# Performance work log

Hardware: AMD Instinct MI355X
Metric: run time of the kernel (lower is better)

Reference implementation:

```python
import jax, jax.numpy as jnp
import numpy as np

T, B, D, H, L = 512, 128, 256, 256, 4
EPS = 1e-5

def _ln(x, g, b):
    m = jnp.mean(x, axis=-1, keepdims=True)
    v = jnp.mean((x - m) ** 2, axis=-1, keepdims=True)
    return (x - m) * jax.lax.rsqrt(v + EPS) * g + b

def setup_inputs() -> dict:
    key = jax.random.key(0)
    ks = jax.random.split(key, 24)
    s = 0.02
    inp = {
        "x": jax.random.normal(ks[0], (T, B, D), dtype=jnp.float32),
        "lengths": jax.random.randint(ks[1], (B,), 1, T + 1, dtype=jnp.int32),
        # LinearEnchancedGRU params
        "Wr": jax.random.normal(ks[2], (D + H, H)) * s,
        "gr": jnp.ones((H,)), "br": jnp.zeros((H,)),
        "Wz": jax.random.normal(ks[3], (D + H, H)) * s,
        "gz": jnp.ones((H,)), "bz": jnp.zeros((H,)),
        "Wl": jax.random.normal(ks[4], (D + H, H)) * s,
        "gl": jnp.ones((H,)), "bl": jnp.zeros((H,)),
        "Wlt": jax.random.normal(ks[5], (D, H)) * s,
        "Cx": jax.random.normal(ks[6], (D, H)) * s,
        "Ch_w": jax.random.normal(ks[7], (H, H)) * s,
        "Ch_b": jnp.zeros((H,)),
        # TransitionGRU stack params [L, ...]
        "tWr": jax.random.normal(ks[8], (L, H, H)) * s,
        "tgr": jnp.ones((L, H)), "tbr": jnp.zeros((L, H)),
        "tWz": jax.random.normal(ks[9], (L, H, H)) * s,
        "tgz": jnp.ones((L, H)), "tbz": jnp.zeros((L, H)),
        "tWc": jax.random.normal(ks[10], (L, H, H)) * s,
        "tbc": jnp.zeros((L, H)),
    }
    return inp

def reference(x, lengths, Wr, gr, br, Wz, gz, bz, Wl, gl, bl, Wlt, Cx, Ch_w, Ch_b,
              tWr, tgr, tbr, tWz, tgz, tbz, tWc, tbc):
    # x: [T,B,D]; lengths: [B]. Packed-sequence semantics: hidden state of a
    # finished example is frozen; its outputs are zero padding.
    mask = jnp.arange(T, dtype=jnp.int32)[:, None] < lengths[None, :]  # [T,B]

    def cell(xt, h):
        cat = jnp.concatenate([xt, h], axis=-1)  # [B, D+H]
        r = jax.nn.sigmoid(_ln(cat @ Wr, gr, br))
        z = jax.nn.sigmoid(_ln(cat @ Wz, gz, bz))
        l = jax.nn.sigmoid(_ln(cat @ Wl, gl, bl))
        n = jnp.tanh(xt @ Cx + r * (h @ Ch_w + Ch_b)) + l * (xt @ Wlt)
        h = (1.0 - z) * h + z * n
        for i in range(L):  # deep transition stack (fixed small depth)
            ri = jax.nn.sigmoid(_ln(h @ tWr[i], tgr[i], tbr[i]))
            zi = jax.nn.sigmoid(_ln(h @ tWz[i], tgz[i], tbz[i]))
            ni = jnp.tanh(ri * (h @ tWc[i] + tbc[i]))
            h = (1.0 - zi) * ni + zi * h
        return h

    def step(h, inputs):
        xt, mt = inputs  # [B,D], [B]
        hn = cell(xt, h)
        hn = jnp.where(mt[:, None], hn, h)
        out = jnp.where(mt[:, None], hn, 0.0)
        return hn, out

    h0 = jnp.zeros((B, H), dtype=x.dtype)
    _, outs = jax.lax.scan(step, h0, (x, mask))  # outs: [T,B,H]
    return outs
```

## Files before the change

### kernel.cpp

```cpp
#include <hip/hip_runtime.h>
#include <hip/hip_bf16.h>

#define T_ 512
#define B_ 128
#define D_ 256
#define H_ 256
#define EPS 1e-5f

typedef __attribute__((ext_vector_type(8))) short short8;
typedef __attribute__((ext_vector_type(4))) short short4v;
typedef __attribute__((ext_vector_type(4))) float f32x4;

#define WT1A_OFF 0
#define WT1B_OFF 393216
#define WT1C_OFF 524288
#define WTT_OFF  589824
#define WTT_PER  196608
#define WT_TOTAL 1376256

#define PRE_OFFB  2752512UL
#define SLOT_OFFB 4325376UL
#define NSLOTS    256

__device__ __forceinline__ short f2bf(float f) {
  unsigned u = __builtin_bit_cast(unsigned, f);
  u = (u + 0x7FFFu + ((u >> 16) & 1u)) >> 16;
  return (short)u;
}

__device__ __forceinline__ f32x4 zero4() { f32x4 z = {0.f, 0.f, 0.f, 0.f}; return z; }

__device__ __forceinline__ f32x4 mfma16(short8 a, short8 b, f32x4 c) {
  return __builtin_amdgcn_mfma_f32_16x16x32_bf16(a, b, c, 0, 0, 0);
}

__device__ __forceinline__ void red2(float& a, float& b) {
  #pragma unroll
  for (int off = 32; off; off >>= 1) {
    a += __shfl_xor(a, off);
    b += __shfl_xor(b, off);
  }
}

__device__ __forceinline__ f32x4 ln_sig(f32x4 v, f32x4 g, f32x4 bb) {
  float s1 = v[0] + v[1] + v[2] + v[3];
  float s2 = v[0]*v[0] + v[1]*v[1] + v[2]*v[2] + v[3]*v[3];
  red2(s1, s2);
  float m = s1 * (1.f / 256.f);
  float var = s2 * (1.f / 256.f) - m * m;
  float rs = rsqrtf((var > 0.f ? var : 0.f) + EPS);
  f32x4 o;
  #pragma unroll
  for (int i = 0; i < 4; ++i) {
    float t = (v[i] - m) * rs * g[i] + bb[i];
    o[i] = 1.f / (1.f + __expf(-t));
  }
  return o;
}

__device__ __forceinline__ f32x4 ald4(float* p) {
  unsigned long long* q = (unsigned long long*)p;
  unsigned long long a = __hip_atomic_load(q,     __ATOMIC_RELAXED, __HIP_MEMORY_SCOPE_AGENT);
  unsigned long long b = __hip_atomic_load(q + 1, __ATOMIC_RELAXED, __HIP_MEMORY_SCOPE_AGENT);
  f32x4 v;
  v[0] = __builtin_bit_cast(float, (unsigned)(a & 0xffffffffu));
  v[1] = __builtin_bit_cast(float, (unsigned)(a >> 32));
  v[2] = __builtin_bit_cast(float, (unsigned)(b & 0xffffffffu));
  v[3] = __builtin_bit_cast(float, (unsigned)(b >> 32));
  return v;
}
__device__ __forceinline__ void ast1(float* p, float v) {
  __hip_atomic_store((unsigned*)p, __builtin_bit_cast(unsigned, v),
                     __ATOMIC_RELAXED, __HIP_MEMORY_SCOPE_AGENT);
}

__global__ void prep_weights(const float* __restrict__ Wr, const float* __restrict__ Wz,
                             const float* __restrict__ Wl, const float* __restrict__ Wlt,
                             const float* __restrict__ Cx, const float* __restrict__ Chw,
                             const float* __restrict__ tWr, const float* __restrict__ tWz,
                             const float* __restrict__ tWc, short* __restrict__ wt) {
  int idx = blockIdx.x * 256 + threadIdx.x;
  if (idx >= WT_TOTAL) return;
  float v;
  if (idx < WT1B_OFF) {
    int n = idx >> 9, k = idx & 511;
    const float* W = (n < 256) ? Wr : (n < 512 ? Wz : Wl);
    v = W[k * 256 + (n & 255)];
  } else if (idx < WT1C_OFF) {
    int r = idx - WT1B_OFF;
    int n = r >> 8, k = r & 255;
    v = (n < 256) ? Cx[k * 256 + n] : Wlt[k * 256 + (n - 256)];
  } else if (idx < WTT_OFF) {
    int r = idx - WT1C_OFF;
    int n = r >> 8, k = r & 255;
    v = Chw[k * 256 + n];
  } else {
    int r = idx - WTT_OFF;
    int i = r / WTT_PER;
    int rr = r - i * WTT_PER;
    int n = rr >> 8, k = rr & 255;
    const float* W = (n < 256) ? tWr : (n < 512 ? tWz : tWc);
    v = W[(i * 256 + k) * 256 + (n & 255)];
  }
  wt[idx] = f2bf(v);
}

__global__ __launch_bounds__(256)
void rnn_cluster(const float* __restrict__ x, const int* __restrict__ lengths,
                 const float* __restrict__ gr, const float* __restrict__ br,
                 const float* __restrict__ gz, const float* __restrict__ bz,
                 const float* __restrict__ gl, const float* __restrict__ bl,
                 const float* __restrict__ Chb,
                 const float* __restrict__ tgr, const float* __restrict__ tbr,
                 const float* __restrict__ tgz, const float* __restrict__ tbz,
                 const float* __restrict__ tbc,
                 const short* __restrict__ W, float* __restrict__ pre,
                 unsigned* __restrict__ slots, float* __restrict__ out) {

  __shared__ __align__(16) char smem[32768];
  char*  HBF = smem;
  char*  XBF = smem + 8192;
  float* HF  = (float*)(smem + 16384);
  __shared__ int wg_dead;

  const int tid = threadIdx.x;
  const int w   = tid >> 6, l = tid & 63;
  const int la  = l & 15, lh = l >> 4;
  const int amask = (la & 7) << 4;
  const int bid = blockIdx.x;
  const int cl  = bid & 7;
  const int sl  = bid >> 3;
  const int rb0 = cl * 16;
  const int c0  = sl * 16;
  const int c0e = 4 * l;

  for (int i = tid; i < 1024; i += 256) ((short4v*)HBF)[i] = (short4v){0, 0, 0, 0};
  for (int i = tid; i < 1024; i += 256) ((f32x4*)HF)[i] = zero4();
  if (tid == 0) wg_dead = 0;

  int maxlen = 0;
  for (int i = 0; i < 16; ++i) {
    int v = lengths[rb0 + i];
    maxlen = maxlen > v ? maxlen : v;
  }
  int lenr[4];
  #pragma unroll
  for (int i = 0; i < 4; ++i) lenr[i] = lengths[rb0 + 4 * w + i];

  unsigned* slotb = slots + cl * 32;

  auto csync = [&](int R) {
    asm volatile("s_waitcnt vmcnt(0)" ::: "memory");
    __syncthreads();
    if (tid == 0)
      __hip_atomic_store(slotb + (R & 1) * 16 + sl, (unsigned)(R + 1),
                         __ATOMIC_RELAXED, __HIP_MEMORY_SCOPE_AGENT);
    if (!wg_dead) {
      unsigned tag = (unsigned)(R + 1);
      unsigned* sp = slotb + (R & 1) * 16 + (l & 15);
      int it = 0;
      while (__hip_atomic_load(sp, __ATOMIC_RELAXED, __HIP_MEMORY_SCOPE_AGENT) < tag) {
        if (++it > 200000) { wg_dead = 1; break; }
        __builtin_amdgcn_s_sleep(2);
      }
    }
    asm volatile("" ::: "memory");
  };

  __syncthreads();

  for (int t = 0; t < maxlen; ++t) {
    {
      const float* xt = x + ((size_t)t * B_ + rb0) * D_;
      for (int c = tid; c < 1024; c += 256) {
        int row = c >> 6, j = c & 63;
        f32x4 v = *(const f32x4*)(xt + row * D_ + 4 * j);
        short4v s = { f2bf(v[0]), f2bf(v[1]), f2bf(v[2]), f2bf(v[3]) };
        *(short4v*)(XBF + row * 512 + ((8 * j) ^ ((row & 7) << 4))) = s;
      }
    }
    __syncthreads();

    int R = t * 5;
    {
      float* P = pre + (size_t)(((R & 1) * 8 + cl) * 6) * 4096;
      if (w < 3) {
        f32x4 acc = zero4();
        const short* bp = W + WT1A_OFF + (size_t)(w * 256 + c0 + la) * 512 + lh * 8;
        #pragma unroll
        for (int kf = 0; kf < 16; ++kf) {
          int aoff = la * 512 + ((((kf & 7) * 64) + lh * 16) ^ amask);
          short8 a = (kf < 8) ? *(const short8*)(XBF + aoff) : *(const short8*)(HBF + aoff);
          acc = mfma16(a, *(const short8*)(bp + kf * 32), acc);
        }
        #pragma unroll
        for (int i = 0; i < 4; ++i) ast1(P + w * 4096 + (lh * 4 + i) * 256 + c0 + la, acc[i]);
      } else {
        f32x4 a0 = zero4(), a1 = zero4(), a2 = zero4();
        const short* b0 = W + WT1B_OFF + (size_t)(c0 + la) * 256 + lh * 8;
        const short* b1 = W + WT1B_OFF + (size_t)(256 + c0 + la) * 256 + lh * 8;
        const short* b2 = W + WT1C_OFF + (size_t)(c0 + la) * 256 + lh * 8;
        #pragma unroll
        for (int kf = 0; kf < 8; ++kf) {
          int aoff = la * 512 + (((kf * 64) + lh * 16) ^ amask);
          short8 ax = *(const short8*)(XBF + aoff);
          short8 ah = *(const short8*)(HBF + aoff);
          a0 = mfma16(ax, *(const short8*)(b0 + kf * 32), a0);
          a1 = mfma16(ax, *(const short8*)(b1 + kf * 32), a1);
          a2 = mfma16(ah, *(const short8*)(b2 + kf * 32), a2);
        }
        #pragma unroll
        for (int i = 0; i < 4; ++i) {
          ast1(P + 3 * 4096 + (lh * 4 + i) * 256 + c0 + la, a0[i]);
          ast1(P + 4 * 4096 + (lh * 4 + i) * 256 + c0 + la, a1[i]);
          ast1(P + 5 * 4096 + (lh * 4 + i) * 256 + c0 + la, a2[i]);
        }
      }
      csync(R);

      f32x4 g4r = *(const f32x4*)(gr + c0e), b4r = *(const f32x4*)(br + c0e);
      f32x4 g4z = *(const f32x4*)(gz + c0e), b4z = *(const f32x4*)(bz + c0e);
      f32x4 g4l = *(const f32x4*)(gl + c0e), b4l = *(const f32x4*)(bl + c0e);
      f32x4 cb4 = *(const f32x4*)(Chb + c0e);
      #pragma unroll
      for (int i = 0; i < 4; ++i) {
        int row = 4 * w + i;
        float* Pr = P + row * 256 + c0e;
        f32x4 pr  = ald4(Pr);
        f32x4 pz  = ald4(Pr + 4096);
        f32x4 pl  = ald4(Pr + 2 * 4096);
        f32x4 xcx = ald4(Pr + 3 * 4096);
        f32x4 xwl = ald4(Pr + 4 * 4096);
        f32x4 hch = ald4(Pr + 5 * 4096);
        f32x4 r4 = ln_sig(pr, g4r, b4r);
        f32x4 z4 = ln_sig(pz, g4z, b4z);
        f32x4 l4 = ln_sig(pl, g4l, b4l);
        f32x4 h = *(const f32x4*)&HF[row * 256 + c0e];
        f32x4 hn;
        #pragma unroll
        for (int q = 0; q < 4; ++q) {
          float n = tanhf(xcx[q] + r4[q] * (hch[q] + cb4[q])) + l4[q] * xwl[q];
          hn[q] = (1.f - z4[q]) * h[q] + z4[q] * n;
        }
        if (t < lenr[i]) {
          *(f32x4*)&HF[row * 256 + c0e] = hn;
          short4v sv = { f2bf(hn[0]), f2bf(hn[1]), f2bf(hn[2]), f2bf(hn[3]) };
          *(short4v*)(HBF + row * 512 + ((8 * l) ^ ((row & 7) << 4))) = sv;
        }
      }
    }
    __syncthreads();

    #pragma unroll 1
    for (int li = 0; li < 4; ++li) {
      R = t * 5 + 1 + li;
      float* P = pre + (size_t)(((R & 1) * 8 + cl) * 6) * 4096;
      if (w < 3) {
        f32x4 acc = zero4();
        const short* bp = W + WTT_OFF + li * WTT_PER + (size_t)(w * 256 + c0 + la) * 256 + lh * 8;
        #pragma unroll
        for (int kf = 0; kf < 8; ++kf) {
          int aoff = la * 512 + (((kf * 64) + lh * 16) ^ amask);
          short8 a = *(const short8*)(HBF + aoff);
          acc = mfma16(a, *(const short8*)(bp + kf * 32), acc);
        }
        #pragma unroll
        for (int i = 0; i < 4; ++i) ast1(P + w * 4096 + (lh * 4 + i) * 256 + c0 + la, acc[i]);
      }
      csync(R);

      f32x4 g4r = *(const f32x4*)(tgr + li * 256 + c0e), b4r = *(const f32x4*)(tbr + li * 256 + c0e);
      f32x4 g4z = *(const f32x4*)(tgz + li * 256 + c0e), b4z = *(const f32x4*)(tbz + li * 256 + c0e);
      f32x4 cb4 = *(const f32x4*)(tbc + li * 256 + c0e);
      #pragma unroll
      for (int i = 0; i < 4; ++i) {
        int row = 4 * w + i;
        float* Pr = P + row * 256 + c0e;
        f32x4 pr = ald4(Pr);
        f32x4 pz = ald4(Pr + 4096);
        f32x4 pc = ald4(Pr + 2 * 4096);
        f32x4 ri = ln_sig(pr, g4r, b4r);
        f32x4 zi = ln_sig(pz, g4z, b4z);
        f32x4 h = *(const f32x4*)&HF[row * 256 + c0e];
        f32x4 hn;
        #pragma unroll
        for (int q = 0; q < 4; ++q) {
          float n = tanhf(ri[q] * (pc[q] + cb4[q]));
          hn[q] = (1.f - zi[q]) * n + zi[q] * h[q];
        }
        bool act = t < lenr[i];
        if (act) {
          *(f32x4*)&HF[row * 256 + c0e] = hn;
          short4v sv = { f2bf(hn[0]), f2bf(hn[1]), f2bf(hn[2]), f2bf(hn[3]) };
          *(short4v*)(HBF + row * 512 + ((8 * l) ^ ((row & 7) << 4))) = sv;
        }
        if (li == 3 && (l >> 2) == sl) {
          f32x4 o = act ? hn : zero4();
          *(f32x4*)(out + ((size_t)t * B_ + rb0 + row) * H_ + c0e) = o;
        }
      }
      __syncthreads();
    }
  }

  for (int t = maxlen; t < T_; ++t) {
    if (tid < 64) {
      int row = tid >> 2, cc = (tid & 3) * 4;
      *(f32x4*)(out + ((size_t)t * B_ + rb0 + row) * H_ + c0 + cc) = zero4();
    }
  }
}

extern "C" void kernel_launch(void* const* d_in, const int* in_sizes, int n_in,
                              void* d_out, int out_size, void* d_ws, size_t ws_size,
                              hipStream_t stream) {
  const float* x    = (const float*)d_in[0];
  const int* lengths = (const int*)d_in[1];
  const float* Wr   = (const float*)d_in[2];
  const float* gr   = (const float*)d_in[3];
  const float* br   = (const float*)d_in[4];
  const float* Wz   = (const float*)d_in[5];
  const float* gz   = (const float*)d_in[6];
  const float* bz   = (const float*)d_in[7];
  const float* Wl   = (const float*)d_in[8];
  const float* gl   = (const float*)d_in[9];
  const float* bl   = (const float*)d_in[10];
  const float* Wlt  = (const float*)d_in[11];
  const float* Cx   = (const float*)d_in[12];
  const float* Chw  = (const float*)d_in[13];
  const float* Chb  = (const float*)d_in[14];
  const float* tWr  = (const float*)d_in[15];
  const float* tgr  = (const float*)d_in[16];
  const float* tbr  = (const float*)d_in[17];
  const float* tWz  = (const float*)d_in[18];
  const float* tgz  = (const float*)d_in[19];
  const float* tbz  = (const float*)d_in[20];
  const float* tWc  = (const float*)d_in[21];
  const float* tbc  = (const float*)d_in[22];

  short*    wt    = (short*)d_ws;
  float*    pre   = (float*)((char*)d_ws + PRE_OFFB);
  unsigned* slots = (unsigned*)((char*)d_ws + SLOT_OFFB);

  hipMemsetAsync(slots, 0, NSLOTS * sizeof(unsigned), stream);
  hipLaunchKernelGGL(prep_weights, dim3((WT_TOTAL + 255) / 256), dim3(256), 0, stream,
                     Wr, Wz, Wl, Wlt, Cx, Chw, tWr, tWz, tWc, wt);
  hipLaunchKernelGGL(rnn_cluster, dim3(128), dim3(256), 0, stream,
                     x, lengths, gr, br, gz, bz, gl, bl, Chb,
                     tgr, tbr, tgz, tbz, tbc, wt, pre, slots, (float*)d_out);
}
```

Baseline: 19.71 ms.

## Use per-wave completion flags and prefetch next-phase weights into registers

Replaces the workgroup barrier plus single per-workgroup flag with per-wave flags: each wave publishes its own slot and consumers poll only the flags they need, skipping the absent fourth wave in transition layers. While waiting, the weight fragments for the next phase's h-dependent matmul are preloaded into registers, taking global weight loads off the critical path. The flag array grows and the spin timeout and sleep change. Register pressure rises, and correctness depends on the finer-grained flag ordering.

```diff
diff --git a/kernel.cpp b/kernel.cpp
--- a/kernel.cpp
+++ b/kernel.cpp
@@ -20,7 +20,7 @@
 
 #define PRE_OFFB  2752512UL
 #define SLOT_OFFB 4325376UL
-#define NSLOTS    256
+#define NSLOTS    1024
 
 __device__ __forceinline__ short f2bf(float f) {
   unsigned u = __builtin_bit_cast(unsigned, f);
@@ -147,25 +147,36 @@
   #pragma unroll
   for (int i = 0; i < 4; ++i) lenr[i] = lengths[rb0 + 4 * w + i];
 
-  unsigned* slotb = slots + cl * 32;
-
-  auto csync = [&](int R) {
-    asm volatile("s_waitcnt vmcnt(0)" ::: "memory");
-    __syncthreads();
-    if (tid == 0)
-      __hip_atomic_store(slotb + (R & 1) * 16 + sl, (unsigned)(R + 1),
-                         __ATOMIC_RELAXED, __HIP_MEMORY_SCOPE_AGENT);
+  unsigned* slotb = slots + cl * 128;
+
+  const short* bgate = W + WT1A_OFF + (size_t)((w < 3 ? w : 0) * 256 + c0 + la) * 512 + lh * 8;
+  const short* b0p   = W + WT1B_OFF + (size_t)(c0 + la) * 256 + lh * 8;
+  const short* b1p   = W + WT1B_OFF + (size_t)(256 + c0 + la) * 256 + lh * 8;
+  const short* b2p   = W + WT1C_OFF + (size_t)(c0 + la) * 256 + lh * 8;
+
+  auto pollflags = [&](int R, bool all4) {
+    unsigned tag = (unsigned)(R + 1);
     if (!wg_dead) {
-      unsigned tag = (unsigned)(R + 1);
-      unsigned* sp = slotb + (R & 1) * 16 + (l & 15);
-      int it = 0;
-      while (__hip_atomic_load(sp, __ATOMIC_RELAXED, __HIP_MEMORY_SCOPE_AGENT) < tag) {
-        if (++it > 200000) { wg_dead = 1; break; }
-        __builtin_amdgcn_s_sleep(2);
+      if (all4 || (l & 3) != 3) {
+        unsigned* sp = slotb + (R & 1) * 64 + l;
+        int it = 0;
+        while (__hip_atomic_load(sp, __ATOMIC_RELAXED, __HIP_MEMORY_SCOPE_AGENT) < tag) {
+          if (++it > 500000) { wg_dead = 1; break; }
+          __builtin_amdgcn_s_sleep(1);
+        }
       }
     }
     asm volatile("" ::: "memory");
   };
+
+  short8 bpre[8];
+  if (w < 3) {
+    #pragma unroll
+    for (int kf = 0; kf < 8; ++kf) bpre[kf] = *(const short8*)(bgate + (8 + kf) * 32);
+  } else {
+    #pragma unroll
+    for (int kf = 0; kf < 8; ++kf) bpre[kf] = *(const short8*)(b2p + kf * 32);
+  }
 
   __syncthreads();
 
@@ -186,28 +197,31 @@
       float* P = pre + (size_t)(((R & 1) * 8 + cl) * 6) * 4096;
       if (w < 3) {
         f32x4 acc = zero4();
-        const short* bp = W + WT1A_OFF + (size_t)(w * 256 + c0 + la) * 512 + lh * 8;
-        #pragma unroll
-        for (int kf = 0; kf < 16; ++kf) {
-          int aoff = la * 512 + ((((kf & 7) * 64) + lh * 16) ^ amask);
-          short8 a = (kf < 8) ? *(const short8*)(XBF + aoff) : *(const short8*)(HBF + aoff);
-          acc = mfma16(a, *(const short8*)(bp + kf * 32), acc);
+        #pragma unroll
+        for (int kf = 0; kf < 8; ++kf) {
+          int aoff = la * 512 + (((kf * 64) + lh * 16) ^ amask);
+          acc = mfma16(*(const short8*)(XBF + aoff), *(const short8*)(bgate + kf * 32), acc);
+        }
+        #pragma unroll
+        for (int kf = 0; kf < 8; ++kf) {
+          int aoff = la * 512 + (((kf * 64) + lh * 16) ^ amask);
+          acc = mfma16(*(const short8*)(HBF + aoff), bpre[kf], acc);
         }
         #pragma unroll
         for (int i = 0; i < 4; ++i) ast1(P + w * 4096 + (lh * 4 + i) * 256 + c0 + la, acc[i]);
       } else {
         f32x4 a0 = zero4(), a1 = zero4(), a2 = zero4();
-        const short* b0 = W + WT1B_OFF + (size_t)(c0 + la) * 256 + lh * 8;
-        const short* b1 = W + WT1B_OFF + (size_t)(256 + c0 + la) * 256 + lh * 8;
-        const short* b2 = W + WT1C_OFF + (size_t)(c0 + la) * 256 + lh * 8;
         #pragma unroll
         for (int kf = 0; kf < 8; ++kf) {
           int aoff = la * 512 + (((kf * 64) + lh * 16) ^ amask);
           short8 ax = *(const short8*)(XBF + aoff);
-          short8 ah = *(const short8*)(HBF + aoff);
-          a0 = mfma16(ax, *(const short8*)(b0 + kf * 32), a0);
-          a1 = mfma16(ax, *(const short8*)(b1 + kf * 32), a1);
-          a2 = mfma16(ah, *(const short8*)(b2 + kf * 32), a2);
+          a0 = mfma16(ax, *(const short8*)(b0p + kf * 32), a0);
+          a1 = mfma16(ax, *(const short8*)(b1p + kf * 32), a1);
+        }
+        #pragma unroll
+        for (int kf = 0; kf < 8; ++kf) {
+          int aoff = la * 512 + (((kf * 64) + lh * 16) ^ amask);
+          a2 = mfma16(*(const short8*)(HBF + aoff), bpre[kf], a2);
         }
         #pragma unroll
         for (int i = 0; i < 4; ++i) {
@@ -216,7 +230,16 @@
           ast1(P + 5 * 4096 + (lh * 4 + i) * 256 + c0 + la, a2[i]);
         }
       }
-      csync(R);
+      asm volatile("s_waitcnt vmcnt(0)" ::: "memory");
+      if (l == 0)
+        __hip_atomic_store(slotb + (R & 1) * 64 + sl * 4 + w, (unsigned)(R + 1),
+                           __ATOMIC_RELAXED, __HIP_MEMORY_SCOPE_AGENT);
+      if (w < 3) {
+        const short* bt = W + WTT_OFF + (size_t)(w * 256 + c0 + la) * 256 + lh * 8;
+        #pragma unroll
+        for (int kf = 0; kf < 8; ++kf) bpre[kf] = *(const short8*)(bt + kf * 32);
+      }
+      pollflags(R, true);
 
       f32x4 g4r = *(const f32x4*)(gr + c0e), b4r = *(const f32x4*)(br + c0e);
       f32x4 g4z = *(const f32x4*)(gz + c0e), b4z = *(const f32x4*)(bz + c0e);
@@ -257,17 +280,34 @@
       float* P = pre + (size_t)(((R & 1) * 8 + cl) * 6) * 4096;
       if (w < 3) {
         f32x4 acc = zero4();
-        const short* bp = W + WTT_OFF + li * WTT_PER + (size_t)(w * 256 + c0 + la) * 256 + lh * 8;
-        #pragma unroll
-        for (int kf = 0; kf < 8; ++kf) {
-          int aoff = la * 512 + (((kf * 64) + lh * 16) ^ amask);
-          short8 a = *(const short8*)(HBF + aoff);
-          acc = mfma16(a, *(const short8*)(bp + kf * 32), acc);
+        #pragma unroll
+        for (int kf = 0; kf < 8; ++kf) {
+          int aoff = la * 512 + (((kf * 64) + lh * 16) ^ amask);
+          acc = mfma16(*(const short8*)(HBF + aoff), bpre[kf], acc);
         }
         #pragma unroll
         for (int i = 0; i < 4; ++i) ast1(P + w * 4096 + (lh * 4 + i) * 256 + c0 + la, acc[i]);
-      }
-      csync(R);
+        asm volatile("s_waitcnt vmcnt(0)" ::: "memory");
+        if (l == 0)
+          __hip_atomic_store(slotb + (R & 1) * 64 + sl * 4 + w, (unsigned)(R + 1),
+                             __ATOMIC_RELAXED, __HIP_MEMORY_SCOPE_AGENT);
+      }
+      if (li < 3) {
+        if (w < 3) {
+          const short* bt = W + WTT_OFF + (li + 1) * WTT_PER + (size_t)(w * 256 + c0 + la) * 256 + lh * 8;
+          #pragma unroll
+          for (int kf = 0; kf < 8; ++kf) bpre[kf] = *(const short8*)(bt + kf * 32);
+        }
+      } else {
+        if (w < 3) {
+          #pragma unroll
+          for (int kf = 0; kf < 8; ++kf) bpre[kf] = *(const short8*)(bgate + (8 + kf) * 32);
+        } else {
+          #pragma unroll
+          for (int kf = 0; kf < 8; ++kf) bpre[kf] = *(const short8*)(b2p + kf * 32);
+        }
+      }
+      pollflags(R, false);
 
       f32x4 g4r = *(const f32x4*)(tgr + li * 256 + c0e), b4r = *(const f32x4*)(tbr + li * 256 + c0e);
       f32x4 g4z = *(const f32x4*)(tgz + li * 256 + c0e), b4z = *(const f32x4*)(tbz + li * 256 + c0e);
```

Result: slower. 22.42 ms (+13.8%).

## Exchange LayerNorm partial stats and bf16 hidden slices instead of full preactivations

Applied to the files above, without the earlier changes.

Replaces the 256-thread-per-block design, which wrote full fp32 preactivations to global memory for cross-block exchange, with a single-wavefront-per-block scheme. Each block keeps its 16-column weight slice resident in LDS and registers, computes the gate products locally, and exchanges only per-row LayerNorm sums and sums of squares plus its bf16 hidden-state slice through global flags. The aim is to cut global traffic and synchronisation latency on every recurrent step. In exchange each step now needs two flag barriers instead of one, and the grid has far fewer threads per block.

```diff
diff --git a/kernel.cpp b/kernel.cpp
--- a/kernel.cpp
+++ b/kernel.cpp
@@ -11,52 +11,32 @@
 typedef __attribute__((ext_vector_type(4))) short short4v;
 typedef __attribute__((ext_vector_type(4))) float f32x4;
 
-#define WT1A_OFF 0
-#define WT1B_OFF 393216
-#define WT1C_OFF 524288
-#define WTT_OFF  589824
-#define WTT_PER  196608
+#define SLICE_E  86016
 #define WT_TOTAL 1376256
 
-#define PRE_OFFB  2752512UL
-#define SLOT_OFFB 4325376UL
-#define NSLOTS    256
+#define STATS_OFFB 2752512UL
+#define HX_OFFB    2850816UL
+#define FLAG_OFFB  2981888UL
+#define NFLAGS     512
+
+#define L_XBF  0
+#define L_HBF  8192
+#define L_G6   16384
+#define L_SRED 22528
+#define L_AUX  23040
+#define L_TRN  47616
+#define L_END  145920
 
 __device__ __forceinline__ short f2bf(float f) {
   unsigned u = __builtin_bit_cast(unsigned, f);
   u = (u + 0x7FFFu + ((u >> 16) & 1u)) >> 16;
   return (short)u;
 }
-
 __device__ __forceinline__ f32x4 zero4() { f32x4 z = {0.f, 0.f, 0.f, 0.f}; return z; }
-
 __device__ __forceinline__ f32x4 mfma16(short8 a, short8 b, f32x4 c) {
   return __builtin_amdgcn_mfma_f32_16x16x32_bf16(a, b, c, 0, 0, 0);
 }
-
-__device__ __forceinline__ void red2(float& a, float& b) {
-  #pragma unroll
-  for (int off = 32; off; off >>= 1) {
-    a += __shfl_xor(a, off);
-    b += __shfl_xor(b, off);
-  }
-}
-
-__device__ __forceinline__ f32x4 ln_sig(f32x4 v, f32x4 g, f32x4 bb) {
-  float s1 = v[0] + v[1] + v[2] + v[3];
-  float s2 = v[0]*v[0] + v[1]*v[1] + v[2]*v[2] + v[3]*v[3];
-  red2(s1, s2);
-  float m = s1 * (1.f / 256.f);
-  float var = s2 * (1.f / 256.f) - m * m;
-  float rs = rsqrtf((var > 0.f ? var : 0.f) + EPS);
-  f32x4 o;
-  #pragma unroll
-  for (int i = 0; i < 4; ++i) {
-    float t = (v[i] - m) * rs * g[i] + bb[i];
-    o[i] = 1.f / (1.f + __expf(-t));
-  }
-  return o;
-}
+__device__ __forceinline__ void waitv0() { asm volatile("s_waitcnt vmcnt(0)" ::: "memory"); }
 
 __device__ __forceinline__ f32x4 ald4(float* p) {
   unsigned long long* q = (unsigned long long*)p;
@@ -69,7 +49,7 @@
   v[3] = __builtin_bit_cast(float, (unsigned)(b >> 32));
   return v;
 }
-__device__ __forceinline__ void ast1(float* p, float v) {
+__device__ __forceinline__ void ast1f(float* p, float v) {
   __hip_atomic_store((unsigned*)p, __builtin_bit_cast(unsigned, v),
                      __ATOMIC_RELAXED, __HIP_MEMORY_SCOPE_AGENT);
 }
@@ -81,234 +61,330 @@
                              const float* __restrict__ tWc, short* __restrict__ wt) {
   int idx = blockIdx.x * 256 + threadIdx.x;
   if (idx >= WT_TOTAL) return;
+  int j  = idx / SLICE_E;
+  int r  = idx - j * SLICE_E;
+  int u  = r >> 12;
+  int rr = r & 4095;
+  int kf = rr >> 9;
+  int le = rr & 511;
+  int l  = le >> 3, e = le & 7;
+  int la = l & 15, lh = l >> 4;
+  int col = j * 16 + la;
   float v;
-  if (idx < WT1B_OFF) {
-    int n = idx >> 9, k = idx & 511;
-    const float* W = (n < 256) ? Wr : (n < 512 ? Wz : Wl);
-    v = W[k * 256 + (n & 255)];
-  } else if (idx < WT1C_OFF) {
-    int r = idx - WT1B_OFF;
-    int n = r >> 8, k = r & 255;
-    v = (n < 256) ? Cx[k * 256 + n] : Wlt[k * 256 + (n - 256)];
-  } else if (idx < WTT_OFF) {
-    int r = idx - WT1C_OFF;
-    int n = r >> 8, k = r & 255;
-    v = Chw[k * 256 + n];
+  if (u < 6) {
+    int g = u >> 1, half = u & 1;
+    int k = half * 256 + lh * 8 + kf * 32 + e;
+    const float* W = (g == 0) ? Wr : (g == 1 ? Wz : Wl);
+    v = W[k * 256 + col];
+  } else if (u < 9) {
+    int a = u - 6;
+    int k = lh * 8 + kf * 32 + e;
+    const float* W = (a == 0) ? Cx : (a == 1 ? Wlt : Chw);
+    v = W[k * 256 + col];
   } else {
-    int r = idx - WTT_OFF;
-    int i = r / WTT_PER;
-    int rr = r - i * WTT_PER;
-    int n = rr >> 8, k = rr & 255;
-    const float* W = (n < 256) ? tWr : (n < 512 ? tWz : tWc);
-    v = W[(i * 256 + k) * 256 + (n & 255)];
+    int q = u - 9;
+    int li = q / 3, m = q - li * 3;
+    int k = lh * 8 + kf * 32 + e;
+    const float* W = (m == 0) ? tWr : (m == 1 ? tWz : tWc);
+    v = W[(li * 256 + k) * 256 + col];
   }
   wt[idx] = f2bf(v);
 }
 
-__global__ __launch_bounds__(256)
-void rnn_cluster(const float* __restrict__ x, const int* __restrict__ lengths,
-                 const float* __restrict__ gr, const float* __restrict__ br,
-                 const float* __restrict__ gz, const float* __restrict__ bz,
-                 const float* __restrict__ gl, const float* __restrict__ bl,
-                 const float* __restrict__ Chb,
-                 const float* __restrict__ tgr, const float* __restrict__ tbr,
-                 const float* __restrict__ tgz, const float* __restrict__ tbz,
-                 const float* __restrict__ tbc,
-                 const short* __restrict__ W, float* __restrict__ pre,
-                 unsigned* __restrict__ slots, float* __restrict__ out) {
-
-  __shared__ __align__(16) char smem[32768];
-  char*  HBF = smem;
-  char*  XBF = smem + 8192;
-  float* HF  = (float*)(smem + 16384);
-  __shared__ int wg_dead;
-
-  const int tid = threadIdx.x;
-  const int w   = tid >> 6, l = tid & 63;
-  const int la  = l & 15, lh = l >> 4;
+__global__ __launch_bounds__(64)
+void rnn_sx(const float* __restrict__ x, const int* __restrict__ lengths,
+            const float* __restrict__ gr, const float* __restrict__ br,
+            const float* __restrict__ gz, const float* __restrict__ bz,
+            const float* __restrict__ gl, const float* __restrict__ bl,
+            const float* __restrict__ Chb,
+            const float* __restrict__ tgr, const float* __restrict__ tbr,
+            const float* __restrict__ tgz, const float* __restrict__ tbz,
+            const float* __restrict__ tbc,
+            const short* __restrict__ W, float* __restrict__ stats,
+            short* __restrict__ hxs, unsigned* __restrict__ flags,
+            float* __restrict__ out) {
+
+  __shared__ __align__(16) char smem[L_END];
+
+  const int l  = threadIdx.x;
+  const int la = l & 15, lh = l >> 4;
   const int amask = (la & 7) << 4;
   const int bid = blockIdx.x;
-  const int cl  = bid & 7;
-  const int sl  = bid >> 3;
+  const int cl = bid & 7, j = bid >> 3;
   const int rb0 = cl * 16;
-  const int c0  = sl * 16;
-  const int c0e = 4 * l;
-
-  for (int i = tid; i < 1024; i += 256) ((short4v*)HBF)[i] = (short4v){0, 0, 0, 0};
-  for (int i = tid; i < 1024; i += 256) ((f32x4*)HF)[i] = zero4();
-  if (tid == 0) wg_dead = 0;
+  const int myrow = l >> 2, mc = (l & 3) * 4;
+  const int cg = j * 16 + mc;
+  const int colb = (l & 3) * 64;
+
+  const short* Wsl = W + (size_t)j * SLICE_E;
+
+  #pragma unroll 1
+  for (int u = 0; u < 15; ++u) {
+    char* dst = smem + ((u < 3) ? (L_AUX + u * 8192) : (L_TRN + (u - 3) * 8192));
+    const short* src = Wsl + (size_t)(u + 6) * 4096;
+    #pragma unroll
+    for (int kf = 0; kf < 8; ++kf)
+      *(short8*)(dst + kf * 1024 + l * 16) = *(const short8*)(src + kf * 512 + l * 8);
+  }
+  for (int i = l; i < 1024; i += 64) ((short4v*)(smem + L_HBF))[i] = (short4v){0, 0, 0, 0};
 
   int maxlen = 0;
   for (int i = 0; i < 16; ++i) {
     int v = lengths[rb0 + i];
     maxlen = maxlen > v ? maxlen : v;
   }
-  int lenr[4];
-  #pragma unroll
-  for (int i = 0; i < 4; ++i) lenr[i] = lengths[rb0 + 4 * w + i];
-
-  unsigned* slotb = slots + cl * 32;
-
-  auto csync = [&](int R) {
-    asm volatile("s_waitcnt vmcnt(0)" ::: "memory");
-    __syncthreads();
-    if (tid == 0)
-      __hip_atomic_store(slotb + (R & 1) * 16 + sl, (unsigned)(R + 1),
+  const int mylen = lengths[rb0 + myrow];
+
+  float* stc = stats + (size_t)(cl * 2) * 1536;
+  short* hxc = hxs + (size_t)(cl * 2) * 4096;
+  unsigned* flc = flags + cl * 64;
+
+  f32x4 hreg = zero4();
+  int dead = 0;
+
+  auto pollf = [&](unsigned* fb, unsigned tag) {
+    if (!dead) {
+      int it = 0;
+      while (true) {
+        unsigned v = tag;
+        if (l < 16) v = __hip_atomic_load(fb + l, __ATOMIC_RELAXED, __HIP_MEMORY_SCOPE_AGENT);
+        if (__all((int)(v >= tag))) break;
+        if (++it > 300000) { dead = 1; break; }
+        __builtin_amdgcn_s_sleep(1);
+      }
+    }
+    asm volatile("" ::: "memory");
+  };
+  auto ldu = [&](short8 (&dst)[8], const short* bp) {
+    #pragma unroll
+    for (int kf = 0; kf < 8; ++kf) dst[kf] = *(const short8*)(bp + kf * 512 + l * 8);
+  };
+  auto mm8r = [&](short8 (&Bv)[8], f32x4& acc, int Ab) {
+    #pragma unroll
+    for (int kf = 0; kf < 8; ++kf) {
+      int aoff = Ab + la * 512 + (((kf * 64) + lh * 16) ^ amask);
+      acc = mfma16(*(const short8*)(smem + aoff), Bv[kf], acc);
+    }
+  };
+  auto mmlds = [&](int Bub, f32x4& acc, int Ab) {
+    #pragma unroll
+    for (int kf = 0; kf < 8; ++kf) {
+      int aoff = Ab + la * 512 + (((kf * 64) + lh * 16) ^ amask);
+      short8 bv = *(const short8*)(smem + Bub + kf * 1024 + l * 16);
+      acc = mfma16(*(const short8*)(smem + aoff), bv, acc);
+    }
+  };
+  auto g6store = [&](int arr, f32x4 acc) {
+    #pragma unroll
+    for (int i = 0; i < 4; ++i)
+      *(float*)(smem + L_G6 + ((arr * 16 + lh * 4 + i) * 16 + la) * 4) = acc[i];
+  };
+  auto readhx = [&](int par) {
+    float* hp = (float*)(hxc + par * 4096 + (l >> 2) * 256 + colb);
+    int row2 = l >> 2;
+    #pragma unroll
+    for (int q2 = 0; q2 < 8; ++q2) {
+      f32x4 v = ald4(hp + q2 * 4);
+      *(f32x4*)(smem + L_HBF + row2 * 512 + ((colb * 2 + q2 * 16) ^ ((row2 & 7) << 4))) = v;
+    }
+  };
+  auto posth = [&](int par) {
+    unsigned long long pk =
+        (unsigned long long)(unsigned short)f2bf(hreg[0]) |
+        ((unsigned long long)(unsigned short)f2bf(hreg[1]) << 16) |
+        ((unsigned long long)(unsigned short)f2bf(hreg[2]) << 32) |
+        ((unsigned long long)(unsigned short)f2bf(hreg[3]) << 48);
+    __hip_atomic_store((unsigned long long*)(hxc + par * 4096 + myrow * 256 + cg), pk,
+                       __ATOMIC_RELAXED, __HIP_MEMORY_SCOPE_AGENT);
+  };
+
+  short8 B0[8], B1[8];
+  ldu(B0, Wsl);
+  ldu(B1, Wsl + 4096);
+
+  for (int t = 0; t < maxlen; ++t) {
+    int R = t * 5, par = R & 1;
+    {
+      const float* xs = x + ((size_t)t * B_ + rb0 + (l >> 2)) * D_ + colb;
+      int row2 = l >> 2;
+      #pragma unroll
+      for (int u2 = 0; u2 < 8; ++u2) {
+        f32x4 a = *(const f32x4*)(xs + u2 * 8);
+        f32x4 b = *(const f32x4*)(xs + u2 * 8 + 4);
+        short8 s;
+        s[0] = f2bf(a[0]); s[1] = f2bf(a[1]); s[2] = f2bf(a[2]); s[3] = f2bf(a[3]);
+        s[4] = f2bf(b[0]); s[5] = f2bf(b[1]); s[6] = f2bf(b[2]); s[7] = f2bf(b[3]);
+        *(short8*)(smem + L_XBF + row2 * 512 + ((colb * 2 + u2 * 16) ^ ((row2 & 7) << 4))) = s;
+      }
+    }
+    f32x4 ac[6];
+    #pragma unroll
+    for (int a2 = 0; a2 < 6; ++a2) ac[a2] = zero4();
+    mm8r(B0, ac[0], L_XBF); ldu(B0, Wsl + 2 * 4096);
+    mm8r(B1, ac[0], L_HBF); ldu(B1, Wsl + 3 * 4096);
+    mm8r(B0, ac[1], L_XBF); ldu(B0, Wsl + 4 * 4096);
+    mm8r(B1, ac[1], L_HBF); ldu(B1, Wsl + 5 * 4096);
+    mm8r(B0, ac[2], L_XBF);
+    mm8r(B1, ac[2], L_HBF);
+    mmlds(L_AUX,         ac[3], L_XBF);
+    mmlds(L_AUX + 8192,  ac[4], L_XBF);
+    mmlds(L_AUX + 16384, ac[5], L_HBF);
+    #pragma unroll
+    for (int a2 = 0; a2 < 6; ++a2) g6store(a2, ac[a2]);
+    f32x4 pv[6];
+    #pragma unroll
+    for (int a2 = 0; a2 < 6; ++a2)
+      pv[a2] = *(const f32x4*)(smem + L_G6 + ((a2 * 16 + myrow) * 16 + mc) * 4);
+    float st[6];
+    #pragma unroll
+    for (int g2 = 0; g2 < 3; ++g2) {
+      f32x4 v = pv[g2];
+      st[2 * g2]     = v[0] + v[1] + v[2] + v[3];
+      st[2 * g2 + 1] = v[0] * v[0] + v[1] * v[1] + v[2] * v[2] + v[3] * v[3];
+    }
+    #pragma unroll
+    for (int s2 = 0; s2 < 6; ++s2) {
+      st[s2] += __shfl_xor(st[s2], 1);
+      st[s2] += __shfl_xor(st[s2], 2);
+    }
+    float* sp = stc + par * 1536;
+    {
+      int k4 = l & 3;
+      ast1f(sp + (k4 * 16 + myrow) * 16 + j, st[k4]);
+      if (k4 < 2) ast1f(sp + ((4 + k4) * 16 + myrow) * 16 + j, st[4 + k4]);
+    }
+    waitv0();
+    if (l == 0)
+      __hip_atomic_store(flc + par * 16 + j, (unsigned)(R + 1),
                          __ATOMIC_RELAXED, __HIP_MEMORY_SCOPE_AGENT);
-    if (!wg_dead) {
-      unsigned tag = (unsigned)(R + 1);
-      unsigned* sp = slotb + (R & 1) * 16 + (l & 15);
-      int it = 0;
-      while (__hip_atomic_load(sp, __ATOMIC_RELAXED, __HIP_MEMORY_SCOPE_AGENT) < tag) {
-        if (++it > 200000) { wg_dead = 1; break; }
-        __builtin_amdgcn_s_sleep(2);
-      }
-    }
-    asm volatile("" ::: "memory");
-  };
-
-  __syncthreads();
-
-  for (int t = 0; t < maxlen; ++t) {
+    pollf(flc + par * 16, (unsigned)(R + 1));
     {
-      const float* xt = x + ((size_t)t * B_ + rb0) * D_;
-      for (int c = tid; c < 1024; c += 256) {
-        int row = c >> 6, j = c & 63;
-        f32x4 v = *(const f32x4*)(xt + row * D_ + 4 * j);
-        short4v s = { f2bf(v[0]), f2bf(v[1]), f2bf(v[2]), f2bf(v[3]) };
-        *(short4v*)(XBF + row * 512 + ((8 * j) ^ ((row & 7) << 4))) = s;
-      }
-    }
-    __syncthreads();
-
-    int R = t * 5;
+      float* q = sp + l * 16;
+      f32x4 a = ald4(q), b = ald4(q + 4), c = ald4(q + 8), d = ald4(q + 12);
+      f32x4 s4 = a + b + c + d;
+      *(float*)(smem + L_SRED + l * 4) = s4[0] + s4[1] + s4[2] + s4[3];
+      if (l < 32) {
+        float* q2 = sp + (64 + l) * 16;
+        f32x4 a2 = ald4(q2), b2 = ald4(q2 + 4), c2 = ald4(q2 + 8), d2 = ald4(q2 + 12);
+        f32x4 t4 = a2 + b2 + c2 + d2;
+        *(float*)(smem + L_SRED + (64 + l) * 4) = t4[0] + t4[1] + t4[2] + t4[3];
+      }
+    }
     {
-      float* P = pre + (size_t)(((R & 1) * 8 + cl) * 6) * 4096;
-      if (w < 3) {
-        f32x4 acc = zero4();
-        const short* bp = W + WT1A_OFF + (size_t)(w * 256 + c0 + la) * 512 + lh * 8;
+      float m3[3], rs3[3];
+      #pragma unroll
+      for (int g2 = 0; g2 < 3; ++g2) {
+        float s1 = *(float*)(smem + L_SRED + ((2 * g2) * 16 + myrow) * 4);
+        float s2 = *(float*)(smem + L_SRED + ((2 * g2 + 1) * 16 + myrow) * 4);
+        float mm = s1 * (1.f / 256.f);
+        float vv = s2 * (1.f / 256.f) - mm * mm;
+        m3[g2] = mm; rs3[g2] = rsqrtf((vv > 0.f ? vv : 0.f) + EPS);
+      }
+      f32x4 g4r = *(const f32x4*)(gr + cg), b4r = *(const f32x4*)(br + cg);
+      f32x4 g4z = *(const f32x4*)(gz + cg), b4z = *(const f32x4*)(bz + cg);
+      f32x4 g4l = *(const f32x4*)(gl + cg), b4l = *(const f32x4*)(bl + cg);
+      f32x4 cb4 = *(const f32x4*)(Chb + cg);
+      bool act = t < mylen;
+      f32x4 hn;
+      #pragma unroll
+      for (int q2 = 0; q2 < 4; ++q2) {
+        float rv = 1.f / (1.f + __expf(-((pv[0][q2] - m3[0]) * rs3[0] * g4r[q2] + b4r[q2])));
+        float zv = 1.f / (1.f + __expf(-((pv[1][q2] - m3[1]) * rs3[1] * g4z[q2] + b4z[q2])));
+        float lv = 1.f / (1.f + __expf(-((pv[2][q2] - m3[2]) * rs3[2] * g4l[q2] + b4l[q2])));
+        float n = tanhf(pv[3][q2] + rv * (pv[5][q2] + cb4[q2])) + lv * pv[4][q2];
+        hn[q2] = (1.f - zv) * hreg[q2] + zv * n;
+      }
+      if (act) hreg = hn;
+    }
+    posth(par);
+    waitv0();
+    if (l == 0)
+      __hip_atomic_store(flc + (2 + par) * 16 + j, (unsigned)(R + 1),
+                         __ATOMIC_RELAXED, __HIP_MEMORY_SCOPE_AGENT);
+    pollf(flc + (2 + par) * 16, (unsigned)(R + 1));
+    readhx(par);
+
+    #pragma unroll 1
+    for (int li = 0; li < 4; ++li) {
+      R = t * 5 + 1 + li; par = R & 1;
+      f32x4 tc0 = zero4(), tc1 = zero4(), tc2 = zero4();
+      mmlds(L_TRN + (li * 3 + 0) * 8192, tc0, L_HBF);
+      mmlds(L_TRN + (li * 3 + 1) * 8192, tc1, L_HBF);
+      mmlds(L_TRN + (li * 3 + 2) * 8192, tc2, L_HBF);
+      g6store(0, tc0); g6store(1, tc1); g6store(2, tc2);
+      f32x4 qv[3];
+      #pragma unroll
+      for (int a2 = 0; a2 < 3; ++a2)
+        qv[a2] = *(const f32x4*)(smem + L_G6 + ((a2 * 16 + myrow) * 16 + mc) * 4);
+      float st4[4];
+      #pragma unroll
+      for (int g2 = 0; g2 < 2; ++g2) {
+        f32x4 v = qv[g2];
+        st4[2 * g2]     = v[0] + v[1] + v[2] + v[3];
+        st4[2 * g2 + 1] = v[0] * v[0] + v[1] * v[1] + v[2] * v[2] + v[3] * v[3];
+      }
+      #pragma unroll
+      for (int s2 = 0; s2 < 4; ++s2) {
+        st4[s2] += __shfl_xor(st4[s2], 1);
+        st4[s2] += __shfl_xor(st4[s2], 2);
+      }
+      float* sp2 = stc + par * 1536;
+      ast1f(sp2 + ((l & 3) * 16 + myrow) * 16 + j, st4[l & 3]);
+      waitv0();
+      if (l == 0)
+        __hip_atomic_store(flc + par * 16 + j, (unsigned)(R + 1),
+                           __ATOMIC_RELAXED, __HIP_MEMORY_SCOPE_AGENT);
+      if (li == 3) {
+        ldu(B0, Wsl);
+        ldu(B1, Wsl + 4096);
+      }
+      pollf(flc + par * 16, (unsigned)(R + 1));
+      {
+        float* q = sp2 + l * 16;
+        f32x4 a = ald4(q), b = ald4(q + 4), c = ald4(q + 8), d = ald4(q + 12);
+        f32x4 s4 = a + b + c + d;
+        *(float*)(smem + L_SRED + l * 4) = s4[0] + s4[1] + s4[2] + s4[3];
+      }
+      bool act = t < mylen;
+      {
+        float m2[2], rs2[2];
         #pragma unroll
-        for (int kf = 0; kf < 16; ++kf) {
-          int aoff = la * 512 + ((((kf & 7) * 64) + lh * 16) ^ amask);
-          short8 a = (kf < 8) ? *(const short8*)(XBF + aoff) : *(const short8*)(HBF + aoff);
-          acc = mfma16(a, *(const short8*)(bp + kf * 32), acc);
+        for (int g2 = 0; g2 < 2; ++g2) {
+          float s1 = *(float*)(smem + L_SRED + ((2 * g2) * 16 + myrow) * 4);
+          float s2 = *(float*)(smem + L_SRED + ((2 * g2 + 1) * 16 + myrow) * 4);
+          float mm = s1 * (1.f / 256.f);
+          float vv = s2 * (1.f / 256.f) - mm * mm;
+          m2[g2] = mm; rs2[g2] = rsqrtf((vv > 0.f ? vv : 0.f) + EPS);
         }
-        #pragma unroll
-        for (int i = 0; i < 4; ++i) ast1(P + w * 4096 + (lh * 4 + i) * 256 + c0 + la, acc[i]);
-      } else {
-        f32x4 a0 = zero4(), a1 = zero4(), a2 = zero4();
-        const short* b0 = W + WT1B_OFF + (size_t)(c0 + la) * 256 + lh * 8;
-        const short* b1 = W + WT1B_OFF + (size_t)(256 + c0 + la) * 256 + lh * 8;
-        const short* b2 = W + WT1C_OFF + (size_t)(c0 + la) * 256 + lh * 8;
-        #pragma unroll
-        for (int kf = 0; kf < 8; ++kf) {
-          int aoff = la * 512 + (((kf * 64) + lh * 16) ^ amask);
-          short8 ax = *(const short8*)(XBF + aoff);
-          short8 ah = *(const short8*)(HBF + aoff);
-          a0 = mfma16(ax, *(const short8*)(b0 + kf * 32), a0);
-          a1 = mfma16(ax, *(const short8*)(b1 + kf * 32), a1);
-          a2 = mfma16(ah, *(const short8*)(b2 + kf * 32), a2);
-        }
-        #pragma unroll
-        for (int i = 0; i < 4; ++i) {
-          ast1(P + 3 * 4096 + (lh * 4 + i) * 256 + c0 + la, a0[i]);
-          ast1(P + 4 * 4096 + (lh * 4 + i) * 256 + c0 + la, a1[i]);
-          ast1(P + 5 * 4096 + (lh * 4 + i) * 256 + c0 + la, a2[i]);
-        }
-      }
-      csync(R);
-
-      f32x4 g4r = *(const f32x4*)(gr + c0e), b4r = *(const f32x4*)(br + c0e);
-      f32x4 g4z = *(const f32x4*)(gz + c0e), b4z = *(const f32x4*)(bz + c0e);
-      f32x4 g4l = *(const f32x4*)(gl + c0e), b4l = *(const f32x4*)(bl + c0e);
-      f32x4 cb4 = *(const f32x4*)(Chb + c0e);
-      #pragma unroll
-      for (int i = 0; i < 4; ++i) {
-        int row = 4 * w + i;
-        float* Pr = P + row * 256 + c0e;
-        f32x4 pr  = ald4(Pr);
-        f32x4 pz  = ald4(Pr + 4096);
-        f32x4 pl  = ald4(Pr + 2 * 4096);
-        f32x4 xcx = ald4(Pr + 3 * 4096);
-        f32x4 xwl = ald4(Pr + 4 * 4096);
-        f32x4 hch = ald4(Pr + 5 * 4096);
-        f32x4 r4 = ln_sig(pr, g4r, b4r);
-        f32x4 z4 = ln_sig(pz, g4z, b4z);
-        f32x4 l4 = ln_sig(pl, g4l, b4l);
-        f32x4 h = *(const f32x4*)&HF[row * 256 + c0e];
+        f32x4 g4r = *(const f32x4*)(tgr + li * 256 + cg), b4r = *(const f32x4*)(tbr + li * 256 + cg);
+        f32x4 g4z = *(const f32x4*)(tgz + li * 256 + cg), b4z = *(const f32x4*)(tbz + li * 256 + cg);
+        f32x4 cb4 = *(const f32x4*)(tbc + li * 256 + cg);
         f32x4 hn;
         #pragma unroll
-        for (int q = 0; q < 4; ++q) {
-          float n = tanhf(xcx[q] + r4[q] * (hch[q] + cb4[q])) + l4[q] * xwl[q];
-          hn[q] = (1.f - z4[q]) * h[q] + z4[q] * n;
+        for (int q2 = 0; q2 < 4; ++q2) {
+          float rv = 1.f / (1.f + __expf(-((qv[0][q2] - m2[0]) * rs2[0] * g4r[q2] + b4r[q2])));
+          float zv = 1.f / (1.f + __expf(-((qv[1][q2] - m2[1]) * rs2[1] * g4z[q2] + b4z[q2])));
+          float n = tanhf(rv * (qv[2][q2] + cb4[q2]));
+          hn[q2] = (1.f - zv) * n + zv * hreg[q2];
         }
-        if (t < lenr[i]) {
-          *(f32x4*)&HF[row * 256 + c0e] = hn;
-          short4v sv = { f2bf(hn[0]), f2bf(hn[1]), f2bf(hn[2]), f2bf(hn[3]) };
-          *(short4v*)(HBF + row * 512 + ((8 * l) ^ ((row & 7) << 4))) = sv;
+        if (act) hreg = hn;
+        if (li == 3) {
+          f32x4 o = act ? hreg : zero4();
+          *(f32x4*)(out + ((size_t)t * B_ + rb0 + myrow) * H_ + cg) = o;
         }
       }
-    }
-    __syncthreads();
-
-    #pragma unroll 1
-    for (int li = 0; li < 4; ++li) {
-      R = t * 5 + 1 + li;
-      float* P = pre + (size_t)(((R & 1) * 8 + cl) * 6) * 4096;
-      if (w < 3) {
-        f32x4 acc = zero4();
-        const short* bp = W + WTT_OFF + li * WTT_PER + (size_t)(w * 256 + c0 + la) * 256 + lh * 8;
-        #pragma unroll
-        for (int kf = 0; kf < 8; ++kf) {
-          int aoff = la * 512 + (((kf * 64) + lh * 16) ^ amask);
-          short8 a = *(const short8*)(HBF + aoff);
-          acc = mfma16(a, *(const short8*)(bp + kf * 32), acc);
-        }
-        #pragma unroll
-        for (int i = 0; i < 4; ++i) ast1(P + w * 4096 + (lh * 4 + i) * 256 + c0 + la, acc[i]);
-      }
-      csync(R);
-
-      f32x4 g4r = *(const f32x4*)(tgr + li * 256 + c0e), b4r = *(const f32x4*)(tbr + li * 256 + c0e);
-      f32x4 g4z = *(const f32x4*)(tgz + li * 256 + c0e), b4z = *(const f32x4*)(tbz + li * 256 + c0e);
-      f32x4 cb4 = *(const f32x4*)(tbc + li * 256 + c0e);
-      #pragma unroll
-      for (int i = 0; i < 4; ++i) {
-        int row = 4 * w + i;
-        float* Pr = P + row * 256 + c0e;
-        f32x4 pr = ald4(Pr);
-        f32x4 pz = ald4(Pr + 4096);
-        f32x4 pc = ald4(Pr + 2 * 4096);
-        f32x4 ri = ln_sig(pr, g4r, b4r);
-        f32x4 zi = ln_sig(pz, g4z, b4z);
-        f32x4 h = *(const f32x4*)&HF[row * 256 + c0e];
-        f32x4 hn;
-        #pragma unroll
-        for (int q = 0; q < 4; ++q) {
-          float n = tanhf(ri[q] * (pc[q] + cb4[q]));
-          hn[q] = (1.f - zi[q]) * n + zi[q] * h[q];
-        }
-        bool act = t < lenr[i];
-        if (act) {
-          *(f32x4*)&HF[row * 256 + c0e] = hn;
-          short4v sv = { f2bf(hn[0]), f2bf(hn[1]), f2bf(hn[2]), f2bf(hn[3]) };
-          *(short4v*)(HBF + row * 512 + ((8 * l) ^ ((row & 7) << 4))) = sv;
-        }
-        if (li == 3 && (l >> 2) == sl) {
-          f32x4 o = act ? hn : zero4();
-          *(f32x4*)(out + ((size_t)t * B_ + rb0 + row) * H_ + c0e) = o;
-        }
-      }
-      __syncthreads();
+      posth(par);
+      waitv0();
+      if (l == 0)
+        __hip_atomic_store(flc + (2 + par) * 16 + j, (unsigned)(R + 1),
+                           __ATOMIC_RELAXED, __HIP_MEMORY_SCOPE_AGENT);
+      pollf(flc + (2 + par) * 16, (unsigned)(R + 1));
+      readhx(par);
     }
   }
 
-  for (int t = maxlen; t < T_; ++t) {
-    if (tid < 64) {
-      int row = tid >> 2, cc = (tid & 3) * 4;
-      *(f32x4*)(out + ((size_t)t * B_ + rb0 + row) * H_ + c0 + cc) = zero4();
-    }
-  }
+  for (int t2 = maxlen; t2 < T_; ++t2)
+    *(f32x4*)(out + ((size_t)t2 * B_ + rb0 + myrow) * H_ + cg) = zero4();
 }
 
 extern "C" void kernel_launch(void* const* d_in, const int* in_sizes, int n_in,
@@ -339,13 +415,14 @@
   const float* tbc  = (const float*)d_in[22];
 
   short*    wt    = (short*)d_ws;
-  float*    pre   = (float*)((char*)d_ws + PRE_OFFB);
-  unsigned* slots = (unsigned*)((char*)d_ws + SLOT_OFFB);
-
-  hipMemsetAsync(slots, 0, NSLOTS * sizeof(unsigned), stream);
+  float*    stats = (float*)((char*)d_ws + STATS_OFFB);
+  short*    hxs   = (short*)((char*)d_ws + HX_OFFB);
+  unsigned* flags = (unsigned*)((char*)d_ws + FLAG_OFFB);
+
+  hipMemsetAsync(flags, 0, NFLAGS * sizeof(unsigned), stream);
   hipLaunchKernelGGL(prep_weights, dim3((WT_TOTAL + 255) / 256), dim3(256), 0, stream,
                      Wr, Wz, Wl, Wlt, Cx, Chw, tWr, tWz, tWc, wt);
-  hipLaunchKernelGGL(rnn_cluster, dim3(128), dim3(256), 0, stream,
+  hipLaunchKernelGGL(rnn_sx, dim3(128), dim3(64), 0, stream,
                      x, lengths, gr, br, gz, bz, gl, bl, Chb,
-                     tgr, tbr, tgz, tbz, tbc, wt, pre, slots, (float*)d_out);
-}
+                     tgr, tbr, tgz, tbz, tbc, wt, stats, hxs, flags, (float*)d_out);
+}
```

New measurement: 17.77 ms (median of 2 runs). 9.8% less time.
